# Optimization experiments

Measured on AMD Instinct MI355X. Metric: run time of the kernel, lower is better.

## Reference

```python
import jax, jax.numpy as jnp
import numpy as np

NUM_CLASSES = 6
HIERARCHY_WEIGHT = 0.2


def _build_class_weights():
    w = np.ones(NUM_CLASSES, dtype=np.float32)
    w[0] = 1.2; w[1] = 1.0; w[2] = 1.1; w[3] = 1.3; w[4] = 1.0; w[5] = 1.1
    return jnp.asarray(w)


def _build_hierarchy_matrix():
    p = np.ones((NUM_CLASSES, NUM_CLASSES), dtype=np.float32)
    p[2, 3] = 0.5; p[3, 2] = 0.5
    p[0, 4] = 0.6; p[4, 0] = 0.6
    p[1, 5] = 0.7; p[5, 1] = 0.7
    p[0, 1] = 1.5; p[1, 0] = 1.5
    p[2, 5] = 1.4; p[5, 2] = 1.4
    return jnp.asarray(p)


def setup_inputs() -> dict:
    key = jax.random.key(0)
    k1, k2 = jax.random.split(key)
    B = 4194304
    predictions = jax.random.normal(k1, (B, NUM_CLASSES), dtype=jnp.float32)
    targets = jax.random.randint(k2, (B,), 0, NUM_CLASSES, dtype=jnp.int64)
    return {
        "predictions": predictions,
        "targets": targets,
        "class_weights": _build_class_weights(),
        "hierarchy_matrix": _build_hierarchy_matrix(),
    }


def reference(predictions, targets, class_weights, hierarchy_matrix):
    B = predictions.shape[0]
    # Weighted cross-entropy, matching torch's weighted-mean reduction:
    # sum_i w[t_i] * nll_i / sum_i w[t_i]
    logp = jax.nn.log_softmax(predictions, axis=-1)            # (B, C)
    nll = -jnp.take_along_axis(logp, targets[:, None], axis=-1)[:, 0]  # (B,)
    w = class_weights[targets]                                  # (B,)
    ce_loss = jnp.sum(w * nll) / jnp.sum(w)

    # Hierarchy penalty: sum_{i, j != t_i} probs[i,j] * penalty[t_i, j] / B
    probs = jax.nn.softmax(predictions, axis=-1)               # (B, C)
    pen = hierarchy_matrix[targets]                             # (B, C) gather of penalty rows
    not_target = 1.0 - jax.nn.one_hot(targets, NUM_CLASSES, dtype=probs.dtype)
    hierarchy_loss = jnp.sum(probs * pen * not_target) / B

    total_loss = ce_loss + HIERARCHY_WEIGHT * hierarchy_loss
    return total_loss, ce_loss, hierarchy_loss
```

## Files before the change

### kernel.cpp

```cpp
#include <hip/hip_runtime.h>

#define NC 6
constexpr float HIER_W = 0.2f;

#define AS1 __attribute__((address_space(1)))
#define AS3 __attribute__((address_space(3)))

#define NITER 8
#define STAGE_WORDS (128 * 6 + 128)

__global__ __launch_bounds__(256) void hloss_main(
    const float* __restrict__ preds,
    const int*   __restrict__ targets,
    const float* __restrict__ cw,
    const float* __restrict__ pen,
    float4* __restrict__ partial)
{
    __shared__ float s_cw[NC];
    __shared__ float s_pen[NC * NC];
    __shared__ float s_stage[4][2][STAGE_WORDS];

    if (threadIdx.x < NC * NC) s_pen[threadIdx.x] = pen[threadIdx.x];
    if (threadIdx.x < NC)      s_cw[threadIdx.x]  = cw[threadIdx.x];
    __syncthreads();

    const int wv   = threadIdx.x >> 6;
    const int lane = threadIdx.x & 63;
    const long long wrow0 = ((long long)blockIdx.x * 4 + wv) * (NITER * 128);

    float* const st0 = &s_stage[wv][0][0];
    float* const st1 = &s_stage[wv][1][0];

    auto STAGE = [&](float* buf, int it) {
        const long long r0 = wrow0 + (long long)it * 128;
        const float* gp = preds + r0 * NC;
        #pragma unroll
        for (int k = 0; k < 3; ++k) {
            __builtin_amdgcn_global_load_lds(
                (const AS1 void*)(gp + k * 256 + lane * 4),
                (AS3 void*)(buf + k * 256), 16, 0, 0);
        }
        const int* gt = targets + r0;
        #pragma unroll
        for (int k = 0; k < 2; ++k) {
            __builtin_amdgcn_global_load_lds(
                (const AS1 void*)(gt + k * 64 + lane),
                (AS3 void*)(buf + 768 + k * 64), 4, 0, 0);
        }
    };

    float a_num = 0.f, a_den = 0.f, a_h = 0.f;

    auto ROW = [&](const float* buf, int rr) {
        const int tr = __float_as_int(buf[768 + rr]);
        float xr[NC], e[NC], s = 0.f;
        #pragma unroll
        for (int j = 0; j < NC; ++j) xr[j] = buf[rr * 6 + j];
        #pragma unroll
        for (int j = 0; j < NC; ++j) { e[j] = __expf(xr[j]); s += e[j]; }
        const float inv = __frcp_rn(s);

        float xt = xr[0];
        #pragma unroll
        for (int j = 1; j < NC; ++j) xt = (tr == j) ? xr[j] : xt;

        const float w = s_cw[tr];
        a_num += w * (__logf(s) - xt);
        a_den += w;

        const float* pr = s_pen + tr * NC;
        float dot = 0.f;
        #pragma unroll
        for (int j = 0; j < NC; ++j) dot += e[j] * pr[j];
        a_h += (dot - __expf(xt)) * inv;
    };

    STAGE(st0, 0);
    STAGE(st1, 1);

    #pragma unroll
    for (int it = 0; it < NITER; ++it) {
        float* buf = (it & 1) ? st1 : st0;
        if (it < NITER - 1) { asm volatile("s_waitcnt vmcnt(5)" ::: "memory"); }
        else                { asm volatile("s_waitcnt vmcnt(0)" ::: "memory"); }
        __builtin_amdgcn_sched_barrier(0);

        ROW(buf, lane);
        ROW(buf, 64 + lane);

        if (it + 2 < NITER) {
            asm volatile("s_waitcnt lgkmcnt(0)" ::: "memory");
            __builtin_amdgcn_sched_barrier(0);
            STAGE(buf, it + 2);
        }
    }

    #pragma unroll
    for (int off = 32; off > 0; off >>= 1) {
        a_num += __shfl_xor(a_num, off);
        a_den += __shfl_xor(a_den, off);
        a_h   += __shfl_xor(a_h,   off);
    }

    __shared__ float red[3][4];
    if (lane == 0) { red[0][wv] = a_num; red[1][wv] = a_den; red[2][wv] = a_h; }
    __syncthreads();
    if (threadIdx.x == 0) {
        float n = 0.f, d = 0.f, h = 0.f;
        #pragma unroll
        for (int i = 0; i < 4; ++i) { n += red[0][i]; d += red[1][i]; h += red[2][i]; }
        partial[blockIdx.x] = make_float4(n, d, h, 0.f);
    }
}

__global__ __launch_bounds__(256) void hloss_reduce(
    const float4* __restrict__ partial,
    float* __restrict__ out, float invB)
{
    const int t = threadIdx.x;
    float4 p0 = partial[t];
    float4 p1 = partial[t + 256];
    float4 p2 = partial[t + 512];
    float4 p3 = partial[t + 768];

    float n = p0.x + p1.x + p2.x + p3.x;
    float d = p0.y + p1.y + p2.y + p3.y;
    float h = p0.z + p1.z + p2.z + p3.z;

    #pragma unroll
    for (int off = 32; off > 0; off >>= 1) {
        n += __shfl_xor(n, off);
        d += __shfl_xor(d, off);
        h += __shfl_xor(h, off);
    }
    __shared__ float red[3][4];
    const int wave = t >> 6;
    const int lane = t & 63;
    if (lane == 0) { red[0][wave] = n; red[1][wave] = d; red[2][wave] = h; }
    __syncthreads();
    if (t == 0) {
        float N = 0.f, D = 0.f, H = 0.f;
        #pragma unroll
        for (int i = 0; i < 4; ++i) { N += red[0][i]; D += red[1][i]; H += red[2][i]; }
        const float ce = N / D;
        const float hh = H * invB;
        out[0] = ce + HIER_W * hh;
        out[1] = ce;
        out[2] = hh;
    }
}

extern "C" void kernel_launch(void* const* d_in, const int* in_sizes, int n_in,
                              void* d_out, int out_size, void* d_ws, size_t ws_size,
                              hipStream_t stream)
{
    const float* preds   = (const float*)d_in[0];
    const int*   targets = (const int*)  d_in[1];
    const float* cw      = (const float*)d_in[2];
    const float* pen     = (const float*)d_in[3];
    float4* partial = (float4*)d_ws;
    float* out = (float*)d_out;

    const int B = in_sizes[1];
    const int blocks = B / 4096;

    hipLaunchKernelGGL(hloss_main, dim3(blocks), dim3(256), 0, stream,
                       preds, targets, cw, pen, partial);
    hipLaunchKernelGGL(hloss_reduce, dim3(1), dim3(256), 0, stream,
                       partial, out, 1.0f / (float)B);
}
```

Before: 26.45 us.

## Deepen LDS staging pipeline to four 64-row buffers per wave

Restructures the per-wave async global-to-LDS staging from two 128-row buffers to four 64-row buffers, with 16 iterations per wave instead of 8. This keeps more loads in flight, aiming to hide memory latency better, and adjusts the vmcnt wait counts to match. Rows per block and per wave are unchanged. The costs are more iterations and a larger share of narrow 4-byte LDS-direct loads, which may cut per-instruction efficiency.

```diff
diff --git a/kernel.cpp b/kernel.cpp
--- a/kernel.cpp
+++ b/kernel.cpp
@@ -6,8 +6,9 @@
 #define AS1 __attribute__((address_space(1)))
 #define AS3 __attribute__((address_space(3)))
 
-#define NITER 8
-#define STAGE_WORDS (128 * 6 + 128)
+#define NITER 16
+#define NBUF 4
+#define BUF_WORDS (64 * 6 + 64)
 
 __global__ __launch_bounds__(256) void hloss_main(
     const float* __restrict__ preds,
@@ -18,7 +19,7 @@
 {
     __shared__ float s_cw[NC];
     __shared__ float s_pen[NC * NC];
-    __shared__ float s_stage[4][2][STAGE_WORDS];
+    __shared__ float s_stage[4][NBUF][BUF_WORDS];
 
     if (threadIdx.x < NC * NC) s_pen[threadIdx.x] = pen[threadIdx.x];
     if (threadIdx.x < NC)      s_cw[threadIdx.x]  = cw[threadIdx.x];
@@ -26,36 +27,30 @@
 
     const int wv   = threadIdx.x >> 6;
     const int lane = threadIdx.x & 63;
-    const long long wrow0 = ((long long)blockIdx.x * 4 + wv) * (NITER * 128);
+    const long long wrow0 = ((long long)blockIdx.x * 4 + wv) * (NITER * 64);
 
-    float* const st0 = &s_stage[wv][0][0];
-    float* const st1 = &s_stage[wv][1][0];
-
-    auto STAGE = [&](float* buf, int it) {
-        const long long r0 = wrow0 + (long long)it * 128;
+    auto STAGE = [&](int bi, int it) {
+        float* buf = &s_stage[wv][bi][0];
+        const long long r0 = wrow0 + (long long)it * 64;
         const float* gp = preds + r0 * NC;
-        #pragma unroll
-        for (int k = 0; k < 3; ++k) {
-            __builtin_amdgcn_global_load_lds(
-                (const AS1 void*)(gp + k * 256 + lane * 4),
-                (AS3 void*)(buf + k * 256), 16, 0, 0);
-        }
+        __builtin_amdgcn_global_load_lds(
+            (const AS1 void*)(gp + lane * 4),  (AS3 void*)(buf),       16, 0, 0);
+        __builtin_amdgcn_global_load_lds(
+            (const AS1 void*)(gp + 256 + lane), (AS3 void*)(buf + 256),  4, 0, 0);
+        __builtin_amdgcn_global_load_lds(
+            (const AS1 void*)(gp + 320 + lane), (AS3 void*)(buf + 320),  4, 0, 0);
         const int* gt = targets + r0;
-        #pragma unroll
-        for (int k = 0; k < 2; ++k) {
-            __builtin_amdgcn_global_load_lds(
-                (const AS1 void*)(gt + k * 64 + lane),
-                (AS3 void*)(buf + 768 + k * 64), 4, 0, 0);
-        }
+        __builtin_amdgcn_global_load_lds(
+            (const AS1 void*)(gt + lane),       (AS3 void*)(buf + 384),  4, 0, 0);
     };
 
     float a_num = 0.f, a_den = 0.f, a_h = 0.f;
 
-    auto ROW = [&](const float* buf, int rr) {
-        const int tr = __float_as_int(buf[768 + rr]);
+    auto ROW = [&](const float* buf) {
+        const int tr = __float_as_int(buf[384 + lane]);
         float xr[NC], e[NC], s = 0.f;
         #pragma unroll
-        for (int j = 0; j < NC; ++j) xr[j] = buf[rr * 6 + j];
+        for (int j = 0; j < NC; ++j) xr[j] = buf[lane * 6 + j];
         #pragma unroll
         for (int j = 0; j < NC; ++j) { e[j] = __expf(xr[j]); s += e[j]; }
         const float inv = __frcp_rn(s);
@@ -75,23 +70,25 @@
         a_h += (dot - __expf(xt)) * inv;
     };
 
-    STAGE(st0, 0);
-    STAGE(st1, 1);
+    STAGE(0, 0); STAGE(1, 1); STAGE(2, 2); STAGE(3, 3);
 
     #pragma unroll
     for (int it = 0; it < NITER; ++it) {
-        float* buf = (it & 1) ? st1 : st0;
-        if (it < NITER - 1) { asm volatile("s_waitcnt vmcnt(5)" ::: "memory"); }
-        else                { asm volatile("s_waitcnt vmcnt(0)" ::: "memory"); }
+        const int rem = (NITER - 1 - it) < 3 ? (NITER - 1 - it) : 3;
+        switch (rem) {
+            case 3: asm volatile("s_waitcnt vmcnt(12)" ::: "memory"); break;
+            case 2: asm volatile("s_waitcnt vmcnt(8)"  ::: "memory"); break;
+            case 1: asm volatile("s_waitcnt vmcnt(4)"  ::: "memory"); break;
+            default: asm volatile("s_waitcnt vmcnt(0)" ::: "memory"); break;
+        }
         __builtin_amdgcn_sched_barrier(0);
 
-        ROW(buf, lane);
-        ROW(buf, 64 + lane);
+        ROW(&s_stage[wv][it & (NBUF - 1)][0]);
 
-        if (it + 2 < NITER) {
+        if (it + NBUF < NITER) {
             asm volatile("s_waitcnt lgkmcnt(0)" ::: "memory");
             __builtin_amdgcn_sched_barrier(0);
-            STAGE(buf, it + 2);
+            STAGE(it & (NBUF - 1), it + NBUF);
         }
     }
 
```

Measured after the change: 26.35 us. No clear change (-0.4%).
